# Optimization experiments

Measured on AMD Instinct MI355X. Metric: run time of the kernel, lower is better.

## Reference

```python
import jax, jax.numpy as jnp
import numpy as np

N = 100000
E = 1600000
F_IN = 512
H1, C1 = 8, 8      # layer-1: 8 heads, 8 dims each (concat -> 64)
H2, C2 = 1, 16     # layer-2: 1 head, num_classes=16
SLOPE = 0.2        # GATConv leaky_relu negative slope


def setup_inputs() -> dict:
    key = jax.random.key(0)
    ks = jax.random.split(key, 10)
    x = jax.random.normal(ks[0], (N, F_IN), dtype=jnp.float32)
    edge_index = jax.random.randint(ks[1], (2, E), 0, N, dtype=jnp.int32)
    s = 0.05
    W1 = jax.random.normal(ks[2], (F_IN, H1 * C1), dtype=jnp.float32) * s
    a1_src = jax.random.normal(ks[3], (H1, C1), dtype=jnp.float32) * s
    a1_dst = jax.random.normal(ks[4], (H1, C1), dtype=jnp.float32) * s
    b1 = jnp.zeros((H1 * C1,), dtype=jnp.float32)
    W2 = jax.random.normal(ks[5], (H1 * C1, H2 * C2), dtype=jnp.float32) * s
    a2_src = jax.random.normal(ks[6], (H2, C2), dtype=jnp.float32) * s
    a2_dst = jax.random.normal(ks[7], (H2, C2), dtype=jnp.float32) * s
    b2 = jnp.zeros((H2 * C2,), dtype=jnp.float32)
    return {"x": x, "edge_index": edge_index, "W1": W1, "a1_src": a1_src,
            "a1_dst": a1_dst, "b1": b1, "W2": W2, "a2_src": a2_src,
            "a2_dst": a2_dst, "b2": b2}


def _gat_conv(h, src, dst, W, a_src, a_dst, b, heads, ch):
    n = h.shape[0]
    hp = (h @ W).reshape(n, heads, ch)                      # [N,H,C]
    al_s = jnp.einsum('nhc,hc->nh', hp, a_src)              # [N,H]
    al_d = jnp.einsum('nhc,hc->nh', hp, a_dst)              # [N,H]
    e = jax.nn.leaky_relu(al_s[src] + al_d[dst], SLOPE)     # [E,H]
    # segment softmax over edges sharing a destination (self-loops guarantee >=1 edge/node)
    emax = jax.lax.stop_gradient(jax.ops.segment_max(e, dst, num_segments=n))
    ee = jnp.exp(e - emax[dst])
    denom = jax.ops.segment_sum(ee, dst, num_segments=n)
    alpha = ee / denom[dst]                                 # [E,H]
    msg = hp[src] * alpha[:, :, None]                       # [E,H,C]
    out = jax.ops.segment_sum(msg, dst, num_segments=n)     # [N,H,C]
    return out.reshape(n, heads * ch) + b


def reference(x, edge_index, W1, a1_src, a1_dst, b1, W2, a2_src, a2_dst, b2):
    n = x.shape[0]
    loops = jnp.arange(n, dtype=edge_index.dtype)           # add_self_loops=True
    src = jnp.concatenate([edge_index[0], loops])
    dst = jnp.concatenate([edge_index[1], loops])
    h = jax.nn.elu(_gat_conv(x, src, dst, W1, a1_src, a1_dst, b1, H1, C1))
    h = _gat_conv(h, src, dst, W2, a2_src, a2_dst, b2, H2, C2)
    return jax.nn.log_softmax(h, axis=1)
```

## Files before the change

### kernel.cpp

```cpp
#include <hip/hip_runtime.h>
#include <hip/hip_bf16.h>

#define N_NODES 100000
#define F_IN    512
#define H1      8
#define C1      8
#define D1      64
#define C2      16
#define SLOPE   0.2f
#define CAP     48
#define PSHIFT  8
#define PPART   391
#define CAPP    5120
#define CHUNK   2048

typedef __bf16 bf16_t;
typedef bf16_t bf16x8 __attribute__((ext_vector_type(8)));
typedef float  f32x4  __attribute__((ext_vector_type(4)));

__global__ __launch_bounds__(256) void wcvt_kernel(
    const float* __restrict__ W, bf16_t* __restrict__ Bt)
{
    int i = blockIdx.x * 256 + threadIdx.x;
    if (i >= 64 * 512) return;
    int nn = i >> 9, k = i & 511;
    Bt[i] = (bf16_t)W[k * 64 + nn];
}

union PgSmem {
    struct {
        int hist[PPART], lofs[PPART], gbase[PPART], cursor[PPART];
        int sdata[512];
        int2 fifo[CHUNK];
    } part;
    bf16_t Bsm[8 * 4 * 64 * 8];
};

__global__ __launch_bounds__(512, 4) void pg_kernel(
    const int* __restrict__ ei, int* __restrict__ pcnt, int2* __restrict__ pfifo,
    const float* __restrict__ X, const bf16_t* __restrict__ Bt,
    const float* __restrict__ a1s, const float* __restrict__ a1d,
    bf16_t* __restrict__ HPb, float* __restrict__ als1, float* __restrict__ ald1,
    int E, int total, int Gg, int n)
{
    __shared__ PgSmem sm;
    const int t = threadIdx.x;

    if ((int)blockIdx.x >= Gg) {
        const int chunk0 = ((int)blockIdx.x - Gg) * CHUNK;

        for (int i = t; i < PPART; i += 512) sm.part.hist[i] = 0;
        __syncthreads();

        int srcs[4], dsts[4];
        const int e0 = chunk0 + t * 4;
        if (e0 + 4 <= E) {
            int4 s = *(const int4*)(ei + e0);
            int4 d = *(const int4*)(ei + E + e0);
            srcs[0]=s.x; srcs[1]=s.y; srcs[2]=s.z; srcs[3]=s.w;
            dsts[0]=d.x; dsts[1]=d.y; dsts[2]=d.z; dsts[3]=d.w;
        } else {
#pragma unroll
            for (int j = 0; j < 4; ++j) {
                int e = e0 + j;
                if (e < E)          { srcs[j] = ei[e]; dsts[j] = ei[E + e]; }
                else if (e < total) { srcs[j] = dsts[j] = e - E; }
                else                { srcs[j] = -1;    dsts[j] = -1; }
            }
        }
#pragma unroll
        for (int j = 0; j < 4; ++j)
            if (dsts[j] >= 0) atomicAdd(&sm.part.hist[dsts[j] >> PSHIFT], 1);
        __syncthreads();

        int hv = (t < PPART) ? sm.part.hist[t] : 0;
        sm.part.sdata[t] = hv;
        __syncthreads();
        for (int off = 1; off < 512; off <<= 1) {
            int x = (t >= off) ? sm.part.sdata[t - off] : 0;
            __syncthreads();
            sm.part.sdata[t] += x;
            __syncthreads();
        }
        if (t < PPART) {
            int lo = sm.part.sdata[t] - hv;
            sm.part.lofs[t]   = lo;
            sm.part.cursor[t] = lo;
            sm.part.gbase[t]  = hv ? atomicAdd(&pcnt[t], hv) : 0;
        }
        __syncthreads();

#pragma unroll
        for (int j = 0; j < 4; ++j) {
            if (dsts[j] >= 0) {
                int p = dsts[j] >> PSHIFT;
                int slot = atomicAdd(&sm.part.cursor[p], 1);
                sm.part.fifo[slot] = make_int2(srcs[j], dsts[j]);
            }
        }
        __syncthreads();

        const int w = t >> 6, lane = t & 63;
        for (int p = w; p < PPART; p += 8) {
            int len = sm.part.hist[p];
            int lo  = sm.part.lofs[p];
            int gb  = sm.part.gbase[p];
            int2* dstp = pfifo + (size_t)p * CAPP;
            for (int j = lane; j < len; j += 64) {
                int g = gb + j;
                if (g < CAPP) dstp[g] = sm.part.fifo[lo + j];
            }
        }
        return;
    }

    const int rowbase = (int)blockIdx.x * 128;
    const int w = t >> 6;
    const int lane = t & 63;

    const int rloc = lane & 15;
    const int koff = (lane >> 4) * 8;

    int grow = rowbase + w * 16 + rloc;
    int growc = (grow < n) ? grow : (n - 1);
    const float* arow = X + (size_t)growc * F_IN + koff;

    f32x4 acc[4];
#pragma unroll
    for (int nt = 0; nt < 4; ++nt) acc[nt] = (f32x4){0.f, 0.f, 0.f, 0.f};

#pragma unroll
    for (int half = 0; half < 2; ++half) {
        for (int i = t; i < 2048; i += 512) {
            int l9 = i & 63;
            int nt = (i >> 6) & 3;
            int ks = i >> 8;
            int row = nt * 16 + (l9 & 15);
            int col = (half * 8 + ks) * 32 + (l9 >> 4) * 8;
            *(bf16x8*)(sm.Bsm + (size_t)i * 8) =
                *(const bf16x8*)(Bt + (size_t)row * F_IN + col);
        }
        __syncthreads();

#pragma unroll 4
        for (int ks = 0; ks < 8; ++ks) {
            int kg = (half * 8 + ks) * 32;
            float4 xa0 = *(const float4*)(arow + kg);
            float4 xa1 = *(const float4*)(arow + kg + 4);
            bf16x8 af;
            af[0]=(bf16_t)xa0.x; af[1]=(bf16_t)xa0.y; af[2]=(bf16_t)xa0.z; af[3]=(bf16_t)xa0.w;
            af[4]=(bf16_t)xa1.x; af[5]=(bf16_t)xa1.y; af[6]=(bf16_t)xa1.z; af[7]=(bf16_t)xa1.w;
#pragma unroll
            for (int nt = 0; nt < 4; ++nt) {
                bf16x8 b = *(const bf16x8*)(sm.Bsm + ((ks * 4 + nt) * 64 + lane) * 8);
                acc[nt] = __builtin_amdgcn_mfma_f32_16x16x32_bf16(af, b, acc[nt], 0, 0, 0);
            }
        }
        __syncthreads();
    }

    const int colg = lane & 15;
    const int quad = lane >> 4;
    const int b    = colg >> 3;
    float cs[4], cd[4];
#pragma unroll
    for (int nt = 0; nt < 4; ++nt) {
        cs[nt] = a1s[nt * 16 + colg];
        cd[nt] = a1d[nt * 16 + colg];
    }

#pragma unroll
    for (int i = 0; i < 4; ++i) {
        int r = rowbase + w * 16 + quad * 4 + i;
        bool ok = r < n;
        if (ok) {
            bf16_t* hr = HPb + (size_t)r * D1;
            hr[colg]      = (bf16_t)acc[0][i];
            hr[16 + colg] = (bf16_t)acc[1][i];
            hr[32 + colg] = (bf16_t)acc[2][i];
            hr[48 + colg] = (bf16_t)acc[3][i];
        }
#pragma unroll
        for (int nt = 0; nt < 4; ++nt) {
            float ps = acc[nt][i] * cs[nt];
            float pd = acc[nt][i] * cd[nt];
            ps += __shfl_xor(ps, 1, 64);  pd += __shfl_xor(pd, 1, 64);
            ps += __shfl_xor(ps, 2, 64);  pd += __shfl_xor(pd, 2, 64);
            ps += __shfl_xor(ps, 4, 64);  pd += __shfl_xor(pd, 4, 64);
            if (ok && (colg & 7) == 0) {
                als1[(size_t)r * 8 + 2 * nt + b] = ps;
                ald1[(size_t)r * 8 + 2 * nt + b] = pd;
            }
        }
    }
}

__global__ __launch_bounds__(512) void place_kernel(
    const int2* __restrict__ pfifo, const int* __restrict__ pcnt,
    int* __restrict__ buckets, int* __restrict__ cnt, int n)
{
    __shared__ int lcnt[1 << PSHIFT];
    const int p = blockIdx.x;
    const int dbase = p << PSHIFT;
    const int nd = min(1 << PSHIFT, n - dbase);
    const int t = threadIdx.x;
    for (int i = t; i < nd; i += 512) lcnt[i] = 0;
    __syncthreads();

    int len = pcnt[p]; if (len > CAPP) len = CAPP;
    const int2* f = pfifo + (size_t)p * CAPP;

    int i = t;
    for (; i + 1536 < len; i += 2048) {
        int2 e0 = f[i], e1 = f[i + 512], e2 = f[i + 1024], e3 = f[i + 1536];
        int s0 = atomicAdd(&lcnt[e0.y - dbase], 1);
        int s1 = atomicAdd(&lcnt[e1.y - dbase], 1);
        int s2 = atomicAdd(&lcnt[e2.y - dbase], 1);
        int s3 = atomicAdd(&lcnt[e3.y - dbase], 1);
        if (s0 < CAP) buckets[(size_t)e0.y * CAP + s0] = e0.x;
        if (s1 < CAP) buckets[(size_t)e1.y * CAP + s1] = e1.x;
        if (s2 < CAP) buckets[(size_t)e2.y * CAP + s2] = e2.x;
        if (s3 < CAP) buckets[(size_t)e3.y * CAP + s3] = e3.x;
    }
    for (; i < len; i += 512) {
        int2 e = f[i];
        int s = atomicAdd(&lcnt[e.y - dbase], 1);
        if (s < CAP) buckets[(size_t)e.y * CAP + s] = e.x;
    }
    __syncthreads();
    for (int i2 = t; i2 < nd; i2 += 512) cnt[dbase + i2] = min(lcnt[i2], CAP);
}

#define AGG1_SEC(G0)                                                        \
    {                                                                       \
        _Pragma("unroll")                                                   \
        for (int j = G0; j < G0 + 8; ++j) {                                 \
            int s = bp[j];                                                  \
            s = (j < m) ? s : 0;           \
            float wgt = wbuf[wv][h][j];                                     \
            float v = (float)hp1[(size_t)s * D1 + lane];                    \
            acc = fmaf(wgt, v, acc);                                        \
        }                                                                   \
    }

__global__ __launch_bounds__(256, 2) void agg1_kernel(
    const bf16_t* __restrict__ hp1,
    const float* __restrict__ als, const float* __restrict__ ald,
    const int* __restrict__ cnt, const int* __restrict__ buckets,
    const float* __restrict__ b1,
    const float* __restrict__ W2,
    const float* __restrict__ a2s, const float* __restrict__ a2d,
    bf16_t* __restrict__ HP2b, float* __restrict__ als2, float* __restrict__ ald2,
    int n)
{
    __shared__ float Wsm[64 * 17];
    __shared__ float wbuf[4][8][50];

    const int t = threadIdx.x;
    for (int i = t; i < 1024; i += 256)
        Wsm[(i >> 4) * 17 + (i & 15)] = W2[i];
    __syncthreads();

    const int wv = t >> 6;
    const int lane = t & 63;
    int node = blockIdx.x * 4 + wv;
    if (node >= n) return;
    node = __builtin_amdgcn_readfirstlane(node);
    const int h = lane >> 3;

    int m = cnt[node]; if (m > CAP) m = CAP;
    m = __builtin_amdgcn_readfirstlane(m);
    const int* bp = buckets + (size_t)node * CAP;
    float ad = ald[node * 8 + h];

    const int jbase = lane & 7;
    float wsum = 0.f;
#pragma unroll
    for (int r = 0; r < 6; ++r) {
        int j = jbase + 8 * r;
        int s = (j < m) ? bp[j] : 0;
        float e = als[s * 8 + h] + ad;
        e = (e > 0.f) ? e : SLOPE * e;
        float wgt = (j < m) ? __expf(e) : 0.f;
        wbuf[wv][h][j] = wgt;
        wsum += wgt;
    }
    wsum += __shfl_xor(wsum, 1, 64);
    wsum += __shfl_xor(wsum, 2, 64);
    wsum += __shfl_xor(wsum, 4, 64);
    const float den = wsum;

    float acc = 0.f;
    AGG1_SEC(0);
    if (m > 8)  AGG1_SEC(8);
    if (m > 16) AGG1_SEC(16);
    if (m > 24) AGG1_SEC(24);
    if (m > 32) AGG1_SEC(32);
    if (m > 40) AGG1_SEC(40);

    float v = acc / den + b1[lane];
    v = (v > 0.f) ? v : (__expf(v) - 1.f);

    const int g2 = lane >> 4, c = lane & 15;
    float o = 0.f;
#pragma unroll
    for (int kk = 0; kk < 16; ++kk) {
        float hk = __shfl(v, g2 * 16 + kk, 64);
        o = fmaf(hk, Wsm[(g2 * 16 + kk) * 17 + c], o);
    }
    o += __shfl_xor(o, 16, 64);
    o += __shfl_xor(o, 32, 64);
    if (g2 == 0) HP2b[(size_t)node * 16 + c] = (bf16_t)o;

    float rs = o * a2s[c];
    float rd = o * a2d[c];
    rs += __shfl_xor(rs, 1, 64);  rd += __shfl_xor(rd, 1, 64);
    rs += __shfl_xor(rs, 2, 64);  rd += __shfl_xor(rd, 2, 64);
    rs += __shfl_xor(rs, 4, 64);  rd += __shfl_xor(rd, 4, 64);
    rs += __shfl_xor(rs, 8, 64);  rd += __shfl_xor(rd, 8, 64);
    if (lane == 0) { als2[node] = rs; ald2[node] = rd; }
}

#define AGG2_SEC(G0)                                                        \
    {                                                                       \
        _Pragma("unroll")                                                   \
        for (int j = G0; j < G0 + 8; ++j) {                                 \
            int s = bp[j];                                                  \
            s = (j < m) ? s : 0;                                            \
            float wgt = wbuf[nib][j];                                       \
            float v = (float)hp2[(size_t)s * 16 + c];                       \
            acc = fmaf(wgt, v, acc);                                        \
        }                                                                   \
    }

__global__ __launch_bounds__(256, 2) void agg2_kernel(
    const bf16_t* __restrict__ hp2,
    const float* __restrict__ als, const float* __restrict__ ald,
    const int* __restrict__ cnt, const int* __restrict__ buckets,
    const float* __restrict__ b2,
    float* __restrict__ out, int n)
{
    __shared__ float wbuf[16][50];
    const int t = threadIdx.x;
    const int nib = t >> 4;
    int node = blockIdx.x * 16 + nib;
    if (node >= n) return;
    const int c = t & 15;

    int m = cnt[node]; if (m > CAP) m = CAP;
    const int* bp = buckets + (size_t)node * CAP;
    float ad = ald[node];

    float wsum = 0.f;
#pragma unroll
    for (int r = 0; r < 3; ++r) {
        int j = c + 16 * r;
        int s = (j < m) ? bp[j] : 0;
        float e = als[s] + ad;
        e = (e > 0.f) ? e : SLOPE * e;
        float wgt = (j < m) ? __expf(e) : 0.f;
        wbuf[nib][j] = wgt;
        wsum += wgt;
    }
    wsum += __shfl_xor(wsum, 1, 16);
    wsum += __shfl_xor(wsum, 2, 16);
    wsum += __shfl_xor(wsum, 4, 16);
    wsum += __shfl_xor(wsum, 8, 16);
    const float den = wsum;

    float acc = 0.f;
    AGG2_SEC(0);
    if (m > 8)  AGG2_SEC(8);
    if (m > 16) AGG2_SEC(16);
    if (m > 24) AGG2_SEC(24);
    if (m > 32) AGG2_SEC(32);
    if (m > 40) AGG2_SEC(40);

    float v = acc / den + b2[c];

    float mx = v;
    mx = fmaxf(mx, __shfl_xor(mx, 8, 16));
    mx = fmaxf(mx, __shfl_xor(mx, 4, 16));
    mx = fmaxf(mx, __shfl_xor(mx, 2, 16));
    mx = fmaxf(mx, __shfl_xor(mx, 1, 16));
    float ex = __expf(v - mx);
    float sum = ex;
    sum += __shfl_xor(sum, 8, 16);
    sum += __shfl_xor(sum, 4, 16);
    sum += __shfl_xor(sum, 2, 16);
    sum += __shfl_xor(sum, 1, 16);
    out[(size_t)node * 16 + c] = v - mx - __logf(sum);
}

extern "C" void kernel_launch(void* const* d_in, const int* in_sizes, int n_in,
                              void* d_out, int out_size, void* d_ws, size_t ws_size,
                              hipStream_t stream)
{
    const float* x      = (const float*)d_in[0];
    const int*   ei     = (const int*)  d_in[1];
    const float* W1     = (const float*)d_in[2];
    const float* a1_src = (const float*)d_in[3];
    const float* a1_dst = (const float*)d_in[4];
    const float* b1     = (const float*)d_in[5];
    const float* W2     = (const float*)d_in[6];
    const float* a2_src = (const float*)d_in[7];
    const float* a2_dst = (const float*)d_in[8];
    const float* b2     = (const float*)d_in[9];
    float* out = (float*)d_out;

    const int N = in_sizes[0] / F_IN;
    const int E = in_sizes[1] / 2;
    const int TOT = E + N;

    char* base = (char*)d_ws;
    size_t off = 0;
    auto carve = [&](size_t bytes) -> char* {
        char* p = base + off;
        off += (bytes + 255) & ~(size_t)255;
        return p;
    };
    bf16_t* hp1b    = (bf16_t*)carve((size_t)N * D1 * 2);
    float*  h1      = (float*) carve((size_t)N * D1 * 4);
    bf16_t* hp2b    = (bf16_t*)carve((size_t)N * 16 * 2);
    float*  als1    = (float*) carve((size_t)N * 8 * 4);
    float*  ald1    = (float*) carve((size_t)N * 8 * 4);
    float*  als2    = (float*) carve((size_t)N * 4);
    float*  ald2    = (float*) carve((size_t)N * 4);
    int*    cnt     = (int*)   carve((size_t)N * 4);
    int*    pcnt    = (int*)   carve((size_t)PPART * 4);
    int*    buckets = (int*)   carve((size_t)N * CAP * 4);
    bf16_t* W1b     = (bf16_t*)carve((size_t)64 * 512 * 2);
    int2*  pfifo   = (int2*)h1;

    const int Gp = (TOT + CHUNK - 1) / CHUNK;
    const int Gg = (N + 127) / 128;

    hipMemsetAsync(pcnt, 0, (size_t)PPART * 4, stream);

    wcvt_kernel<<<128, 256, 0, stream>>>(W1, W1b);

    pg_kernel<<<Gg + Gp, 512, 0, stream>>>(ei, pcnt, pfifo,
                                           x, W1b, a1_src, a1_dst,
                                           hp1b, als1, ald1,
                                           E, TOT, Gg, N);

    place_kernel<<<PPART, 512, 0, stream>>>(pfifo, pcnt, buckets, cnt, N);

    agg1_kernel<<<(N + 3) / 4, 256, 0, stream>>>(hp1b, als1, ald1, cnt, buckets,
                                                 b1, W2, a2_src, a2_dst,
                                                 hp2b, als2, ald2, N);

    agg2_kernel<<<(N + 15) / 16, 256, 0, stream>>>(hp2b, als2, ald2, cnt, buckets, b2, out, N);
}
```

Measured before the change: 464.8 us.

## Aggregate directly from partition FIFOs with shared-memory atomics, dropping bucket placement

Removes the place_kernel and per-node bucket arrays. Both aggregation kernels now process each 256-destination partition's edge FIFO in one block and accumulate weighted messages and softmax denominators into LDS with atomics, then apply the epilogue per node. This avoids writing and re-reading the bucket array and the per-node CAP truncation. In exchange, only 391 blocks run, LDS atomic contention goes up, and per-block shared memory is large (about 74KB for layer 1), which limits occupancy.

```diff
diff --git a/kernel.cpp b/kernel.cpp
--- a/kernel.cpp
+++ b/kernel.cpp
@@ -8,7 +8,6 @@
 #define D1      64
 #define C2      16
 #define SLOPE   0.2f
-#define CAP     48
 #define PSHIFT  8
 #define PPART   391
 #define CAPP    5120
@@ -195,201 +194,156 @@
     }
 }
 
-__global__ __launch_bounds__(512) void place_kernel(
-    const int2* __restrict__ pfifo, const int* __restrict__ pcnt,
-    int* __restrict__ buckets, int* __restrict__ cnt, int n)
-{
-    __shared__ int lcnt[1 << PSHIFT];
-    const int p = blockIdx.x;
-    const int dbase = p << PSHIFT;
-    const int nd = min(1 << PSHIFT, n - dbase);
-    const int t = threadIdx.x;
-    for (int i = t; i < nd; i += 512) lcnt[i] = 0;
-    __syncthreads();
-
-    int len = pcnt[p]; if (len > CAPP) len = CAPP;
-    const int2* f = pfifo + (size_t)p * CAPP;
-
-    int i = t;
-    for (; i + 1536 < len; i += 2048) {
-        int2 e0 = f[i], e1 = f[i + 512], e2 = f[i + 1024], e3 = f[i + 1536];
-        int s0 = atomicAdd(&lcnt[e0.y - dbase], 1);
-        int s1 = atomicAdd(&lcnt[e1.y - dbase], 1);
-        int s2 = atomicAdd(&lcnt[e2.y - dbase], 1);
-        int s3 = atomicAdd(&lcnt[e3.y - dbase], 1);
-        if (s0 < CAP) buckets[(size_t)e0.y * CAP + s0] = e0.x;
-        if (s1 < CAP) buckets[(size_t)e1.y * CAP + s1] = e1.x;
-        if (s2 < CAP) buckets[(size_t)e2.y * CAP + s2] = e2.x;
-        if (s3 < CAP) buckets[(size_t)e3.y * CAP + s3] = e3.x;
-    }
-    for (; i < len; i += 512) {
-        int2 e = f[i];
-        int s = atomicAdd(&lcnt[e.y - dbase], 1);
-        if (s < CAP) buckets[(size_t)e.y * CAP + s] = e.x;
-    }
-    __syncthreads();
-    for (int i2 = t; i2 < nd; i2 += 512) cnt[dbase + i2] = min(lcnt[i2], CAP);
-}
-
-#define AGG1_SEC(G0)                                                        \
-    {                                                                       \
-        _Pragma("unroll")                                                   \
-        for (int j = G0; j < G0 + 8; ++j) {                                 \
-            int s = bp[j];                                                  \
-            s = (j < m) ? s : 0;           \
-            float wgt = wbuf[wv][h][j];                                     \
-            float v = (float)hp1[(size_t)s * D1 + lane];                    \
-            acc = fmaf(wgt, v, acc);                                        \
-        }                                                                   \
-    }
-
-__global__ __launch_bounds__(256, 2) void agg1_kernel(
+__global__ __launch_bounds__(512, 2) void sagg1_kernel(
     const bf16_t* __restrict__ hp1,
     const float* __restrict__ als, const float* __restrict__ ald,
-    const int* __restrict__ cnt, const int* __restrict__ buckets,
+    const int* __restrict__ pcnt, const int2* __restrict__ pfifo,
     const float* __restrict__ b1,
     const float* __restrict__ W2,
     const float* __restrict__ a2s, const float* __restrict__ a2d,
     bf16_t* __restrict__ HP2b, float* __restrict__ als2, float* __restrict__ ald2,
     int n)
 {
+    __shared__ float accs[256][64];
+    __shared__ float dens[256][8];
     __shared__ float Wsm[64 * 17];
-    __shared__ float wbuf[4][8][50];
-
+
+    const int p = blockIdx.x;
+    const int dbase = p << PSHIFT;
+    const int nd = min(1 << PSHIFT, n - dbase);
     const int t = threadIdx.x;
-    for (int i = t; i < 1024; i += 256)
-        Wsm[(i >> 4) * 17 + (i & 15)] = W2[i];
+    const int wv = t >> 6, lane = t & 63, h = lane >> 3;
+
+    for (int i = t; i < 256 * 64; i += 512) ((float*)accs)[i] = 0.f;
+    for (int i = t; i < 256 * 8;  i += 512) ((float*)dens)[i] = 0.f;
+    for (int i = t; i < 1024; i += 512) Wsm[(i >> 4) * 17 + (i & 15)] = W2[i];
     __syncthreads();
 
-    const int wv = t >> 6;
-    const int lane = t & 63;
-    int node = blockIdx.x * 4 + wv;
-    if (node >= n) return;
-    node = __builtin_amdgcn_readfirstlane(node);
-    const int h = lane >> 3;
-
-    int m = cnt[node]; if (m > CAP) m = CAP;
-    m = __builtin_amdgcn_readfirstlane(m);
-    const int* bp = buckets + (size_t)node * CAP;
-    float ad = ald[node * 8 + h];
-
-    const int jbase = lane & 7;
-    float wsum = 0.f;
-#pragma unroll
-    for (int r = 0; r < 6; ++r) {
-        int j = jbase + 8 * r;
-        int s = (j < m) ? bp[j] : 0;
-        float e = als[s * 8 + h] + ad;
-        e = (e > 0.f) ? e : SLOPE * e;
-        float wgt = (j < m) ? __expf(e) : 0.f;
-        wbuf[wv][h][j] = wgt;
-        wsum += wgt;
-    }
-    wsum += __shfl_xor(wsum, 1, 64);
-    wsum += __shfl_xor(wsum, 2, 64);
-    wsum += __shfl_xor(wsum, 4, 64);
-    const float den = wsum;
-
-    float acc = 0.f;
-    AGG1_SEC(0);
-    if (m > 8)  AGG1_SEC(8);
-    if (m > 16) AGG1_SEC(16);
-    if (m > 24) AGG1_SEC(24);
-    if (m > 32) AGG1_SEC(32);
-    if (m > 40) AGG1_SEC(40);
-
-    float v = acc / den + b1[lane];
-    v = (v > 0.f) ? v : (__expf(v) - 1.f);
-
-    const int g2 = lane >> 4, c = lane & 15;
-    float o = 0.f;
-#pragma unroll
-    for (int kk = 0; kk < 16; ++kk) {
-        float hk = __shfl(v, g2 * 16 + kk, 64);
-        o = fmaf(hk, Wsm[(g2 * 16 + kk) * 17 + c], o);
-    }
-    o += __shfl_xor(o, 16, 64);
-    o += __shfl_xor(o, 32, 64);
-    if (g2 == 0) HP2b[(size_t)node * 16 + c] = (bf16_t)o;
-
-    float rs = o * a2s[c];
-    float rd = o * a2d[c];
-    rs += __shfl_xor(rs, 1, 64);  rd += __shfl_xor(rd, 1, 64);
-    rs += __shfl_xor(rs, 2, 64);  rd += __shfl_xor(rd, 2, 64);
-    rs += __shfl_xor(rs, 4, 64);  rd += __shfl_xor(rd, 4, 64);
-    rs += __shfl_xor(rs, 8, 64);  rd += __shfl_xor(rd, 8, 64);
-    if (lane == 0) { als2[node] = rs; ald2[node] = rd; }
+    int len = pcnt[p]; if (len > CAPP) len = CAPP;
+    const int2* f = pfifo + (size_t)p * CAPP;
+    const float* aldp = ald + (size_t)dbase * 8;
+
+    for (int base = wv * 64; base < len; base += 512) {
+        int j = base + lane;
+        int2 e = (j < len) ? f[j] : make_int2(0, dbase - 1);
+        int mysrc = e.x;
+        int mydst = e.y - dbase;
+#pragma unroll 2
+        for (int g = 0; g < 64; g += 8) {
+            float vv[8], ww[8];
+            int dl[8];
+#pragma unroll
+            for (int u = 0; u < 8; ++u) {
+                int src = __shfl(mysrc, g + u, 64);
+                int d   = __shfl(mydst, g + u, 64);
+                bool ok = d >= 0;
+                d = ok ? d : 0;
+                dl[u] = d;
+                vv[u] = (float)hp1[(size_t)src * D1 + lane];
+                float e2 = als[src * 8 + h] + aldp[d * 8 + h];
+                e2 = (e2 > 0.f) ? e2 : SLOPE * e2;
+                ww[u] = ok ? __expf(e2) : 0.f;
+            }
+#pragma unroll
+            for (int u = 0; u < 8; ++u) {
+                atomicAdd(&accs[dl[u]][lane], ww[u] * vv[u]);
+                if ((lane & 7) == 0) atomicAdd(&dens[dl[u]][h], ww[u]);
+            }
+        }
+    }
+    __syncthreads();
+
+    for (int d = wv; d < nd; d += 8) {
+        const int node = dbase + d;
+        float v = accs[d][lane] / dens[d][h] + b1[lane];
+        v = (v > 0.f) ? v : (__expf(v) - 1.f);
+
+        const int g2 = lane >> 4, c = lane & 15;
+        float o = 0.f;
+#pragma unroll
+        for (int kk = 0; kk < 16; ++kk) {
+            float hk = __shfl(v, g2 * 16 + kk, 64);
+            o = fmaf(hk, Wsm[(g2 * 16 + kk) * 17 + c], o);
+        }
+        o += __shfl_xor(o, 16, 64);
+        o += __shfl_xor(o, 32, 64);
+        if (g2 == 0) HP2b[(size_t)node * 16 + c] = (bf16_t)o;
+
+        float rs = o * a2s[c];
+        float rd = o * a2d[c];
+        rs += __shfl_xor(rs, 1, 64);  rd += __shfl_xor(rd, 1, 64);
+        rs += __shfl_xor(rs, 2, 64);  rd += __shfl_xor(rd, 2, 64);
+        rs += __shfl_xor(rs, 4, 64);  rd += __shfl_xor(rd, 4, 64);
+        rs += __shfl_xor(rs, 8, 64);  rd += __shfl_xor(rd, 8, 64);
+        if (lane == 0) { als2[node] = rs; ald2[node] = rd; }
+    }
 }
 
-#define AGG2_SEC(G0)                                                        \
-    {                                                                       \
-        _Pragma("unroll")                                                   \
-        for (int j = G0; j < G0 + 8; ++j) {                                 \
-            int s = bp[j];                                                  \
-            s = (j < m) ? s : 0;                                            \
-            float wgt = wbuf[nib][j];                                       \
-            float v = (float)hp2[(size_t)s * 16 + c];                       \
-            acc = fmaf(wgt, v, acc);                                        \
-        }                                                                   \
-    }
-
-__global__ __launch_bounds__(256, 2) void agg2_kernel(
+__global__ __launch_bounds__(512, 2) void sagg2_kernel(
     const bf16_t* __restrict__ hp2,
     const float* __restrict__ als, const float* __restrict__ ald,
-    const int* __restrict__ cnt, const int* __restrict__ buckets,
+    const int* __restrict__ pcnt, const int2* __restrict__ pfifo,
     const float* __restrict__ b2,
     float* __restrict__ out, int n)
 {
-    __shared__ float wbuf[16][50];
+    __shared__ float acc2[256][16];
+    __shared__ float den2[256];
+    __shared__ float aldS[256];
+
+    const int p = blockIdx.x;
+    const int dbase = p << PSHIFT;
+    const int nd = min(1 << PSHIFT, n - dbase);
     const int t = threadIdx.x;
-    const int nib = t >> 4;
-    int node = blockIdx.x * 16 + nib;
-    if (node >= n) return;
-    const int c = t & 15;
-
-    int m = cnt[node]; if (m > CAP) m = CAP;
-    const int* bp = buckets + (size_t)node * CAP;
-    float ad = ald[node];
-
-    float wsum = 0.f;
-#pragma unroll
-    for (int r = 0; r < 3; ++r) {
-        int j = c + 16 * r;
-        int s = (j < m) ? bp[j] : 0;
-        float e = als[s] + ad;
-        e = (e > 0.f) ? e : SLOPE * e;
-        float wgt = (j < m) ? __expf(e) : 0.f;
-        wbuf[nib][j] = wgt;
-        wsum += wgt;
-    }
-    wsum += __shfl_xor(wsum, 1, 16);
-    wsum += __shfl_xor(wsum, 2, 16);
-    wsum += __shfl_xor(wsum, 4, 16);
-    wsum += __shfl_xor(wsum, 8, 16);
-    const float den = wsum;
-
-    float acc = 0.f;
-    AGG2_SEC(0);
-    if (m > 8)  AGG2_SEC(8);
-    if (m > 16) AGG2_SEC(16);
-    if (m > 24) AGG2_SEC(24);
-    if (m > 32) AGG2_SEC(32);
-    if (m > 40) AGG2_SEC(40);
-
-    float v = acc / den + b2[c];
-
-    float mx = v;
-    mx = fmaxf(mx, __shfl_xor(mx, 8, 16));
-    mx = fmaxf(mx, __shfl_xor(mx, 4, 16));
-    mx = fmaxf(mx, __shfl_xor(mx, 2, 16));
-    mx = fmaxf(mx, __shfl_xor(mx, 1, 16));
-    float ex = __expf(v - mx);
-    float sum = ex;
-    sum += __shfl_xor(sum, 8, 16);
-    sum += __shfl_xor(sum, 4, 16);
-    sum += __shfl_xor(sum, 2, 16);
-    sum += __shfl_xor(sum, 1, 16);
-    out[(size_t)node * 16 + c] = v - mx - __logf(sum);
+    const int wv = t >> 6, lane = t & 63;
+    const int u = lane >> 4, c = lane & 15;
+
+    for (int i = t; i < 256 * 16; i += 512) ((float*)acc2)[i] = 0.f;
+    for (int i = t; i < 256; i += 512) den2[i] = 0.f;
+    for (int i = t; i < nd; i += 512) aldS[i] = ald[dbase + i];
+    __syncthreads();
+
+    int len = pcnt[p]; if (len > CAPP) len = CAPP;
+    const int2* f = pfifo + (size_t)p * CAPP;
+
+    for (int base = wv * 64; base < len; base += 512) {
+        int j = base + lane;
+        int2 e = (j < len) ? f[j] : make_int2(0, dbase - 1);
+        int mysrc = e.x;
+        int mydst = e.y - dbase;
+#pragma unroll 4
+        for (int g = 0; g < 64; g += 4) {
+            int idx = g + u;
+            int src = __shfl(mysrc, idx, 64);
+            int d   = __shfl(mydst, idx, 64);
+            bool ok = d >= 0;
+            d = ok ? d : 0;
+            float v = (float)hp2[(size_t)src * 16 + c];
+            float e2 = als[src] + aldS[d];
+            e2 = (e2 > 0.f) ? e2 : SLOPE * e2;
+            float w = ok ? __expf(e2) : 0.f;
+            atomicAdd(&acc2[d][c], w * v);
+            if (c == 0) atomicAdd(&den2[d], w);
+        }
+    }
+    __syncthreads();
+
+    const int grp = t >> 4;
+    const int c2 = t & 15;
+    for (int d = grp; d < nd; d += 32) {
+        float v = acc2[d][c2] / den2[d] + b2[c2];
+        float mx = v;
+        mx = fmaxf(mx, __shfl_xor(mx, 8, 16));
+        mx = fmaxf(mx, __shfl_xor(mx, 4, 16));
+        mx = fmaxf(mx, __shfl_xor(mx, 2, 16));
+        mx = fmaxf(mx, __shfl_xor(mx, 1, 16));
+        float ex = __expf(v - mx);
+        float sum = ex;
+        sum += __shfl_xor(sum, 8, 16);
+        sum += __shfl_xor(sum, 4, 16);
+        sum += __shfl_xor(sum, 2, 16);
+        sum += __shfl_xor(sum, 1, 16);
+        out[(size_t)(dbase + d) * 16 + c2] = v - mx - __logf(sum);
+    }
 }
 
 extern "C" void kernel_launch(void* const* d_in, const int* in_sizes, int n_in,
@@ -420,17 +374,14 @@
         return p;
     };
     bf16_t* hp1b    = (bf16_t*)carve((size_t)N * D1 * 2);
-    float*  h1      = (float*) carve((size_t)N * D1 * 4);
+    int2*   pfifo   = (int2*)  carve((size_t)PPART * CAPP * 8);
     bf16_t* hp2b    = (bf16_t*)carve((size_t)N * 16 * 2);
     float*  als1    = (float*) carve((size_t)N * 8 * 4);
     float*  ald1    = (float*) carve((size_t)N * 8 * 4);
     float*  als2    = (float*) carve((size_t)N * 4);
     float*  ald2    = (float*) carve((size_t)N * 4);
-    int*    cnt     = (int*)   carve((size_t)N * 4);
     int*    pcnt    = (int*)   carve((size_t)PPART * 4);
-    int*    buckets = (int*)   carve((size_t)N * CAP * 4);
     bf16_t* W1b     = (bf16_t*)carve((size_t)64 * 512 * 2);
-    int2*  pfifo   = (int2*)h1;
 
     const int Gp = (TOT + CHUNK - 1) / CHUNK;
     const int Gg = (N + 127) / 128;
@@ -444,11 +395,10 @@
                                            hp1b, als1, ald1,
                                            E, TOT, Gg, N);
 
-    place_kernel<<<PPART, 512, 0, stream>>>(pfifo, pcnt, buckets, cnt, N);
-
-    agg1_kernel<<<(N + 3) / 4, 256, 0, stream>>>(hp1b, als1, ald1, cnt, buckets,
-                                                 b1, W2, a2_src, a2_dst,
-                                                 hp2b, als2, ald2, N);
-
-    agg2_kernel<<<(N + 15) / 16, 256, 0, stream>>>(hp2b, als2, ald2, cnt, buckets, b2, out, N);
+    sagg1_kernel<<<PPART, 512, 0, stream>>>(hp1b, als1, ald1, pcnt, pfifo,
+                                            b1, W2, a2_src, a2_dst,
+                                            hp2b, als2, ald2, N);
+
+    sagg2_kernel<<<PPART, 512, 0, stream>>>(hp2b, als2, ald2, pcnt, pfifo,
+                                            b2, out, N);
 }
```

Measured after the change: 1.499 ms. +222.5%, slower.

## Fuse bucket placement into aggregation kernels using shared-memory per-partition buckets

Applied to the files above, without the earlier changes.

Removes the separate place kernel and the global buckets/cnt arrays. Each aggregation kernel now runs one block per 256-node partition, rebuilds that partition's neighbor lists in LDS from the partition FIFO, and then aggregates the nodes from LDS. This saves the global bucket write and read traffic and one launch. In exchange the bucketing is done twice (once per layer), the grid shrinks to 391 blocks of 512 threads, and about 50KB of LDS per block limits occupancy.

```diff
diff --git a/kernel.cpp b/kernel.cpp
--- a/kernel.cpp
+++ b/kernel.cpp
@@ -195,201 +195,196 @@
     }
 }
 
-__global__ __launch_bounds__(512) void place_kernel(
-    const int2* __restrict__ pfifo, const int* __restrict__ pcnt,
-    int* __restrict__ buckets, int* __restrict__ cnt, int n)
-{
-    __shared__ int lcnt[1 << PSHIFT];
-    const int p = blockIdx.x;
-    const int dbase = p << PSHIFT;
-    const int nd = min(1 << PSHIFT, n - dbase);
-    const int t = threadIdx.x;
-    for (int i = t; i < nd; i += 512) lcnt[i] = 0;
-    __syncthreads();
-
-    int len = pcnt[p]; if (len > CAPP) len = CAPP;
-    const int2* f = pfifo + (size_t)p * CAPP;
-
-    int i = t;
-    for (; i + 1536 < len; i += 2048) {
-        int2 e0 = f[i], e1 = f[i + 512], e2 = f[i + 1024], e3 = f[i + 1536];
-        int s0 = atomicAdd(&lcnt[e0.y - dbase], 1);
-        int s1 = atomicAdd(&lcnt[e1.y - dbase], 1);
-        int s2 = atomicAdd(&lcnt[e2.y - dbase], 1);
-        int s3 = atomicAdd(&lcnt[e3.y - dbase], 1);
-        if (s0 < CAP) buckets[(size_t)e0.y * CAP + s0] = e0.x;
-        if (s1 < CAP) buckets[(size_t)e1.y * CAP + s1] = e1.x;
-        if (s2 < CAP) buckets[(size_t)e2.y * CAP + s2] = e2.x;
-        if (s3 < CAP) buckets[(size_t)e3.y * CAP + s3] = e3.x;
-    }
-    for (; i < len; i += 512) {
-        int2 e = f[i];
-        int s = atomicAdd(&lcnt[e.y - dbase], 1);
-        if (s < CAP) buckets[(size_t)e.y * CAP + s] = e.x;
-    }
-    __syncthreads();
-    for (int i2 = t; i2 < nd; i2 += 512) cnt[dbase + i2] = min(lcnt[i2], CAP);
-}
-
-#define AGG1_SEC(G0)                                                        \
+#define P1SEC(G0)                                                           \
     {                                                                       \
         _Pragma("unroll")                                                   \
         for (int j = G0; j < G0 + 8; ++j) {                                 \
-            int s = bp[j];                                                  \
-            s = (j < m) ? s : 0;           \
+            int s = lbuck[d][j];                                            \
+            s = (j < m) ? s : 0;                                            \
             float wgt = wbuf[wv][h][j];                                     \
             float v = (float)hp1[(size_t)s * D1 + lane];                    \
             acc = fmaf(wgt, v, acc);                                        \
         }                                                                   \
     }
 
-__global__ __launch_bounds__(256, 2) void agg1_kernel(
+__global__ __launch_bounds__(512, 2) void pagg1_kernel(
     const bf16_t* __restrict__ hp1,
     const float* __restrict__ als, const float* __restrict__ ald,
-    const int* __restrict__ cnt, const int* __restrict__ buckets,
+    const int* __restrict__ pcnt, const int2* __restrict__ pfifo,
     const float* __restrict__ b1,
     const float* __restrict__ W2,
     const float* __restrict__ a2s, const float* __restrict__ a2d,
     bf16_t* __restrict__ HP2b, float* __restrict__ als2, float* __restrict__ ald2,
     int n)
 {
+    __shared__ int   lcnt[256];
+    __shared__ int   lbuck[256][CAP];
     __shared__ float Wsm[64 * 17];
-    __shared__ float wbuf[4][8][50];
-
+    __shared__ float wbuf[8][8][50];
+
+    const int p = blockIdx.x;
+    const int dbase = p << PSHIFT;
+    const int nd = min(1 << PSHIFT, n - dbase);
     const int t = threadIdx.x;
-    for (int i = t; i < 1024; i += 256)
-        Wsm[(i >> 4) * 17 + (i & 15)] = W2[i];
+    const int wv = t >> 6, lane = t & 63, h = lane >> 3;
+
+    for (int i = t; i < 256; i += 512) lcnt[i] = 0;
+    for (int i = t; i < 1024; i += 512) Wsm[(i >> 4) * 17 + (i & 15)] = W2[i];
     __syncthreads();
 
-    const int wv = t >> 6;
-    const int lane = t & 63;
-    int node = blockIdx.x * 4 + wv;
-    if (node >= n) return;
-    node = __builtin_amdgcn_readfirstlane(node);
-    const int h = lane >> 3;
-
-    int m = cnt[node]; if (m > CAP) m = CAP;
-    m = __builtin_amdgcn_readfirstlane(m);
-    const int* bp = buckets + (size_t)node * CAP;
-    float ad = ald[node * 8 + h];
-
-    const int jbase = lane & 7;
-    float wsum = 0.f;
-#pragma unroll
-    for (int r = 0; r < 6; ++r) {
-        int j = jbase + 8 * r;
-        int s = (j < m) ? bp[j] : 0;
-        float e = als[s * 8 + h] + ad;
-        e = (e > 0.f) ? e : SLOPE * e;
-        float wgt = (j < m) ? __expf(e) : 0.f;
-        wbuf[wv][h][j] = wgt;
-        wsum += wgt;
-    }
-    wsum += __shfl_xor(wsum, 1, 64);
-    wsum += __shfl_xor(wsum, 2, 64);
-    wsum += __shfl_xor(wsum, 4, 64);
-    const float den = wsum;
-
-    float acc = 0.f;
-    AGG1_SEC(0);
-    if (m > 8)  AGG1_SEC(8);
-    if (m > 16) AGG1_SEC(16);
-    if (m > 24) AGG1_SEC(24);
-    if (m > 32) AGG1_SEC(32);
-    if (m > 40) AGG1_SEC(40);
-
-    float v = acc / den + b1[lane];
-    v = (v > 0.f) ? v : (__expf(v) - 1.f);
-
-    const int g2 = lane >> 4, c = lane & 15;
-    float o = 0.f;
-#pragma unroll
-    for (int kk = 0; kk < 16; ++kk) {
-        float hk = __shfl(v, g2 * 16 + kk, 64);
-        o = fmaf(hk, Wsm[(g2 * 16 + kk) * 17 + c], o);
-    }
-    o += __shfl_xor(o, 16, 64);
-    o += __shfl_xor(o, 32, 64);
-    if (g2 == 0) HP2b[(size_t)node * 16 + c] = (bf16_t)o;
-
-    float rs = o * a2s[c];
-    float rd = o * a2d[c];
-    rs += __shfl_xor(rs, 1, 64);  rd += __shfl_xor(rd, 1, 64);
-    rs += __shfl_xor(rs, 2, 64);  rd += __shfl_xor(rd, 2, 64);
-    rs += __shfl_xor(rs, 4, 64);  rd += __shfl_xor(rd, 4, 64);
-    rs += __shfl_xor(rs, 8, 64);  rd += __shfl_xor(rd, 8, 64);
-    if (lane == 0) { als2[node] = rs; ald2[node] = rd; }
+    int len = pcnt[p]; if (len > CAPP) len = CAPP;
+    const int2* f = pfifo + (size_t)p * CAPP;
+    for (int i = t; i < len; i += 512) {
+        int2 e = f[i];
+        int d = e.y - dbase;
+        int s = atomicAdd(&lcnt[d], 1);
+        if (s < CAP) lbuck[d][s] = e.x;
+    }
+    __syncthreads();
+
+    for (int d = wv; d < nd; d += 8) {
+        const int node = dbase + d;
+        int m = lcnt[d]; if (m > CAP) m = CAP;
+        float ad = ald[node * 8 + h];
+
+        const int jbase = lane & 7;
+        float wsum = 0.f;
+#pragma unroll
+        for (int r = 0; r < 6; ++r) {
+            int j = jbase + 8 * r;
+            int s = (j < m) ? lbuck[d][j] : 0;
+            float e = als[s * 8 + h] + ad;
+            e = (e > 0.f) ? e : SLOPE * e;
+            float wgt = (j < m) ? __expf(e) : 0.f;
+            wbuf[wv][h][j] = wgt;
+            wsum += wgt;
+        }
+        wsum += __shfl_xor(wsum, 1, 64);
+        wsum += __shfl_xor(wsum, 2, 64);
+        wsum += __shfl_xor(wsum, 4, 64);
+        const float den = wsum;
+
+        float acc = 0.f;
+        P1SEC(0);
+        if (m > 8)  P1SEC(8);
+        if (m > 16) P1SEC(16);
+        if (m > 24) P1SEC(24);
+        if (m > 32) P1SEC(32);
+        if (m > 40) P1SEC(40);
+
+        float v = acc / den + b1[lane];
+        v = (v > 0.f) ? v : (__expf(v) - 1.f);
+
+        const int g2 = lane >> 4, c = lane & 15;
+        float o = 0.f;
+#pragma unroll
+        for (int kk = 0; kk < 16; ++kk) {
+            float hk = __shfl(v, g2 * 16 + kk, 64);
+            o = fmaf(hk, Wsm[(g2 * 16 + kk) * 17 + c], o);
+        }
+        o += __shfl_xor(o, 16, 64);
+        o += __shfl_xor(o, 32, 64);
+        if (g2 == 0) HP2b[(size_t)node * 16 + c] = (bf16_t)o;
+
+        float rs = o * a2s[c];
+        float rd = o * a2d[c];
+        rs += __shfl_xor(rs, 1, 64);  rd += __shfl_xor(rd, 1, 64);
+        rs += __shfl_xor(rs, 2, 64);  rd += __shfl_xor(rd, 2, 64);
+        rs += __shfl_xor(rs, 4, 64);  rd += __shfl_xor(rd, 4, 64);
+        rs += __shfl_xor(rs, 8, 64);  rd += __shfl_xor(rd, 8, 64);
+        if (lane == 0) { als2[node] = rs; ald2[node] = rd; }
+    }
 }
 
-#define AGG2_SEC(G0)                                                        \
+#define P2SEC(G0)                                                           \
     {                                                                       \
         _Pragma("unroll")                                                   \
         for (int j = G0; j < G0 + 8; ++j) {                                 \
-            int s = bp[j];                                                  \
+            int s = lbuck[d][j];                                            \
             s = (j < m) ? s : 0;                                            \
-            float wgt = wbuf[nib][j];                                       \
+            float wgt = wbuf2[grp][j];                                      \
             float v = (float)hp2[(size_t)s * 16 + c];                       \
             acc = fmaf(wgt, v, acc);                                        \
         }                                                                   \
     }
 
-__global__ __launch_bounds__(256, 2) void agg2_kernel(
+__global__ __launch_bounds__(512, 2) void pagg2_kernel(
     const bf16_t* __restrict__ hp2,
     const float* __restrict__ als, const float* __restrict__ ald,
-    const int* __restrict__ cnt, const int* __restrict__ buckets,
+    const int* __restrict__ pcnt, const int2* __restrict__ pfifo,
     const float* __restrict__ b2,
     float* __restrict__ out, int n)
 {
-    __shared__ float wbuf[16][50];
+    __shared__ int   lcnt[256];
+    __shared__ int   lbuck[256][CAP];
+    __shared__ float wbuf2[32][50];
+    __shared__ float aldS[256];
+
+    const int p = blockIdx.x;
+    const int dbase = p << PSHIFT;
+    const int nd = min(1 << PSHIFT, n - dbase);
     const int t = threadIdx.x;
-    const int nib = t >> 4;
-    int node = blockIdx.x * 16 + nib;
-    if (node >= n) return;
-    const int c = t & 15;
-
-    int m = cnt[node]; if (m > CAP) m = CAP;
-    const int* bp = buckets + (size_t)node * CAP;
-    float ad = ald[node];
-
-    float wsum = 0.f;
-#pragma unroll
-    for (int r = 0; r < 3; ++r) {
-        int j = c + 16 * r;
-        int s = (j < m) ? bp[j] : 0;
-        float e = als[s] + ad;
-        e = (e > 0.f) ? e : SLOPE * e;
-        float wgt = (j < m) ? __expf(e) : 0.f;
-        wbuf[nib][j] = wgt;
-        wsum += wgt;
-    }
-    wsum += __shfl_xor(wsum, 1, 16);
-    wsum += __shfl_xor(wsum, 2, 16);
-    wsum += __shfl_xor(wsum, 4, 16);
-    wsum += __shfl_xor(wsum, 8, 16);
-    const float den = wsum;
-
-    float acc = 0.f;
-    AGG2_SEC(0);
-    if (m > 8)  AGG2_SEC(8);
-    if (m > 16) AGG2_SEC(16);
-    if (m > 24) AGG2_SEC(24);
-    if (m > 32) AGG2_SEC(32);
-    if (m > 40) AGG2_SEC(40);
-
-    float v = acc / den + b2[c];
-
-    float mx = v;
-    mx = fmaxf(mx, __shfl_xor(mx, 8, 16));
-    mx = fmaxf(mx, __shfl_xor(mx, 4, 16));
-    mx = fmaxf(mx, __shfl_xor(mx, 2, 16));
-    mx = fmaxf(mx, __shfl_xor(mx, 1, 16));
-    float ex = __expf(v - mx);
-    float sum = ex;
-    sum += __shfl_xor(sum, 8, 16);
-    sum += __shfl_xor(sum, 4, 16);
-    sum += __shfl_xor(sum, 2, 16);
-    sum += __shfl_xor(sum, 1, 16);
-    out[(size_t)node * 16 + c] = v - mx - __logf(sum);
+    const int grp = t >> 4, c = t & 15;
+
+    for (int i = t; i < 256; i += 512) lcnt[i] = 0;
+    for (int i = t; i < nd; i += 512) aldS[i] = ald[dbase + i];
+    __syncthreads();
+
+    int len = pcnt[p]; if (len > CAPP) len = CAPP;
+    const int2* f = pfifo + (size_t)p * CAPP;
+    for (int i = t; i < len; i += 512) {
+        int2 e = f[i];
+        int d = e.y - dbase;
+        int s = atomicAdd(&lcnt[d], 1);
+        if (s < CAP) lbuck[d][s] = e.x;
+    }
+    __syncthreads();
+
+    for (int d = grp; d < nd; d += 32) {
+        const int node = dbase + d;
+        int m = lcnt[d]; if (m > CAP) m = CAP;
+        float ad = aldS[d];
+
+        float wsum = 0.f;
+#pragma unroll
+        for (int r = 0; r < 3; ++r) {
+            int j = c + 16 * r;
+            int s = (j < m) ? lbuck[d][j] : 0;
+            float e = als[s] + ad;
+            e = (e > 0.f) ? e : SLOPE * e;
+            float wgt = (j < m) ? __expf(e) : 0.f;
+            wbuf2[grp][j] = wgt;
+            wsum += wgt;
+        }
+        wsum += __shfl_xor(wsum, 1, 16);
+        wsum += __shfl_xor(wsum, 2, 16);
+        wsum += __shfl_xor(wsum, 4, 16);
+        wsum += __shfl_xor(wsum, 8, 16);
+        const float den = wsum;
+
+        float acc = 0.f;
+        P2SEC(0);
+        if (m > 8)  P2SEC(8);
+        if (m > 16) P2SEC(16);
+        if (m > 24) P2SEC(24);
+        if (m > 32) P2SEC(32);
+        if (m > 40) P2SEC(40);
+
+        float v = acc / den + b2[c];
+
+        float mx = v;
+        mx = fmaxf(mx, __shfl_xor(mx, 8, 16));
+        mx = fmaxf(mx, __shfl_xor(mx, 4, 16));
+        mx = fmaxf(mx, __shfl_xor(mx, 2, 16));
+        mx = fmaxf(mx, __shfl_xor(mx, 1, 16));
+        float ex = __expf(v - mx);
+        float sum = ex;
+        sum += __shfl_xor(sum, 8, 16);
+        sum += __shfl_xor(sum, 4, 16);
+        sum += __shfl_xor(sum, 2, 16);
+        sum += __shfl_xor(sum, 1, 16);
+        out[(size_t)node * 16 + c] = v - mx - __logf(sum);
+    }
 }
 
 extern "C" void kernel_launch(void* const* d_in, const int* in_sizes, int n_in,
@@ -420,17 +415,14 @@
         return p;
     };
     bf16_t* hp1b    = (bf16_t*)carve((size_t)N * D1 * 2);
-    float*  h1      = (float*) carve((size_t)N * D1 * 4);
+    int2*   pfifo   = (int2*)  carve((size_t)PPART * CAPP * 8);
     bf16_t* hp2b    = (bf16_t*)carve((size_t)N * 16 * 2);
     float*  als1    = (float*) carve((size_t)N * 8 * 4);
     float*  ald1    = (float*) carve((size_t)N * 8 * 4);
     float*  als2    = (float*) carve((size_t)N * 4);
     float*  ald2    = (float*) carve((size_t)N * 4);
-    int*    cnt     = (int*)   carve((size_t)N * 4);
     int*    pcnt    = (int*)   carve((size_t)PPART * 4);
-    int*    buckets = (int*)   carve((size_t)N * CAP * 4);
     bf16_t* W1b     = (bf16_t*)carve((size_t)64 * 512 * 2);
-    int2*  pfifo   = (int2*)h1;
 
     const int Gp = (TOT + CHUNK - 1) / CHUNK;
     const int Gg = (N + 127) / 128;
@@ -444,11 +436,10 @@
                                            hp1b, als1, ald1,
                                            E, TOT, Gg, N);
 
-    place_kernel<<<PPART, 512, 0, stream>>>(pfifo, pcnt, buckets, cnt, N);
-
-    agg1_kernel<<<(N + 3) / 4, 256, 0, stream>>>(hp1b, als1, ald1, cnt, buckets,
-                                                 b1, W2, a2_src, a2_dst,
-                                                 hp2b, als2, ald2, N);
-
-    agg2_kernel<<<(N + 15) / 16, 256, 0, stream>>>(hp2b, als2, ald2, cnt, buckets, b2, out, N);
+    pagg1_kernel<<<PPART, 512, 0, stream>>>(hp1b, als1, ald1, pcnt, pfifo,
+                                            b1, W2, a2_src, a2_dst,
+                                            hp2b, als2, ald2, N);
+
+    pagg2_kernel<<<PPART, 512, 0, stream>>>(hp2b, als2, ald2, pcnt, pfifo,
+                                            b2, out, N);
 }
```

Measured after the change: 473.4 us. About the same (+1.9%).
